# Performance work log

Hardware: AMD Instinct MI355X
Metric: run time of the kernel (lower is better)

Reference implementation:

```python
import jax, jax.numpy as jnp
import numpy as np

EPS = 1e-12  # torch F.normalize eps

def _l2norm(v, axis):
    n = jnp.sqrt(jnp.sum(v * v, axis=axis, keepdims=True))
    return v / jnp.maximum(n, EPS)

def setup_inputs() -> dict:
    key = jax.random.key(0)
    k1, k2, k3 = jax.random.split(key, 3)
    x = jax.random.normal(k1, (32, 512, 30, 40), dtype=jnp.float32)
    conv_w = jax.random.normal(k2, (64, 512), dtype=jnp.float32) * 0.05
    centroids = jax.random.uniform(k3, (64, 512), dtype=jnp.float32)
    return {"x": x, "conv_w": conv_w, "centroids": centroids}

def reference(x, conv_w, centroids):
    N, C, H, W = x.shape
    K = conv_w.shape[0]
    # descriptor-wise L2 normalization over channel dim
    xn = _l2norm(x, axis=1)
    xf = xn.reshape(N, C, H * W)                      # [N, C, HW]
    # 1x1 conv (no bias) -> soft assignment over clusters
    logits = jnp.einsum('kc,nch->nkh', conv_w, xf)     # [N, K, HW]
    a = jax.nn.softmax(logits, axis=1)
    # fused VLAD: sum_hw a*(x - centroid) = (a @ x^T) - centroid * sum_hw a
    vlad = jnp.einsum('nkh,nch->nkc', a, xf) - a.sum(axis=-1)[..., None] * centroids[None]
    vlad = _l2norm(vlad, axis=2)                      # intra-normalization
    v = vlad.reshape(N, K * C)
    return _l2norm(v, axis=1)
```

## Files before the change

kernel.cpp:

```cpp
#include <hip/hip_runtime.h>
#include <hip/hip_bf16.h>
#include <math.h>

#define N_B   32
#define C_DIM 512
#define K_DIM 64
#define HW    1200
#define PTILE 32
#define NPT   38
#define ASLOT 40

typedef __attribute__((ext_vector_type(8))) short bf16x8;
typedef __attribute__((ext_vector_type(4))) float f32x4;

static __device__ inline short f2bf(float f) {
  __hip_bfloat16 h = __float2bfloat16(f);
  union { __hip_bfloat16 b; short s; } u; u.b = h; return u.s;
}

__global__ __launch_bounds__(256) void k1_logits_softmax(
    const float* __restrict__ x, const float* __restrict__ w,
    unsigned short* __restrict__ a_out, float* __restrict__ asum_part)
{
  __shared__ bf16x8 wlds[64 * 8];
  __shared__ bf16x8 xlds[32 * 8];
  __shared__ float  slog[64 * 36];
  __shared__ float  sred[8 * 32];
  __shared__ float  pinv[32], pmax[32], psum[32];

  const int tid  = threadIdx.x;
  const int lane = tid & 63;
  const int wv   = tid >> 6;
  const int n    = blockIdx.x / NPT;
  const int tile = blockIdx.x % NPT;
  const int p0   = tile * PTILE;

  const int sp = tid & 31;
  const int sg = tid >> 5;
  const bool spv = (p0 + sp) < HW;

  const int lr = lane & 15;
  const int lg = lane >> 4;

  const float* xb = x + (size_t)n * C_DIM * HW;

  f32x4 acc0 = {0.f, 0.f, 0.f, 0.f};
  f32x4 acc1 = {0.f, 0.f, 0.f, 0.f};
  float ssq = 0.f;

  for (int c0 = 0; c0 < C_DIM; c0 += 64) {
    {
      const int k = tid >> 3, o = tid & 7;
#pragma unroll
      for (int i = 0; i < 2; ++i) {
        const int kk = k + 32 * i;
        const float* wp = w + (size_t)kk * C_DIM + c0 + o * 8;
        float4 w0 = *(const float4*)wp;
        float4 w1 = *(const float4*)(wp + 4);
        bf16x8 v;
        v[0]=f2bf(w0.x); v[1]=f2bf(w0.y); v[2]=f2bf(w0.z); v[3]=f2bf(w0.w);
        v[4]=f2bf(w1.x); v[5]=f2bf(w1.y); v[6]=f2bf(w1.z); v[7]=f2bf(w1.w);
        wlds[kk * 8 + o] = v;
      }
    }
    {
      float f[8];
#pragma unroll
      for (int j = 0; j < 8; ++j) {
        float v = spv ? xb[(size_t)(c0 + sg * 8 + j) * HW + p0 + sp] : 0.f;
        ssq += v * v;
        f[j] = v;
      }
      bf16x8 v;
#pragma unroll
      for (int j = 0; j < 8; ++j) v[j] = f2bf(f[j]);
      xlds[sp * 8 + sg] = v;
    }
    __syncthreads();
    {
      const int kw = wv * 16;
#pragma unroll
      for (int kc = 0; kc < 2; ++kc) {
        bf16x8 af = wlds[(kw + lr) * 8 + kc * 4 + lg];
        bf16x8 b0 = xlds[lr * 8 + kc * 4 + lg];
        bf16x8 b1 = xlds[(16 + lr) * 8 + kc * 4 + lg];
        acc0 = __builtin_amdgcn_mfma_f32_16x16x32_bf16(af, b0, acc0, 0, 0, 0);
        acc1 = __builtin_amdgcn_mfma_f32_16x16x32_bf16(af, b1, acc1, 0, 0, 0);
      }
    }
    __syncthreads();
  }

  sred[sg * 32 + sp] = ssq;
  __syncthreads();
  if (tid < 32) {
    float s = 0.f;
#pragma unroll
    for (int g = 0; g < 8; ++g) s += sred[g * 32 + tid];
    pinv[tid] = 1.f / fmaxf(sqrtf(s), 1e-12f);
  }
  __syncthreads();

  {
    const int kw = wv * 16;
    const float i0 = pinv[lr];
    const float i1 = pinv[16 + lr];
#pragma unroll
    for (int r = 0; r < 4; ++r) {
      slog[(kw + lg * 4 + r) * 36 + lr]      = acc0[r] * i0;
      slog[(kw + lg * 4 + r) * 36 + 16 + lr] = acc1[r] * i1;
    }
  }
  __syncthreads();

  {
    const int p = tid & 31;
    const int kg = tid >> 5;
    float e[8];
    float m = -1e30f;
#pragma unroll
    for (int j = 0; j < 8; ++j) { e[j] = slog[(kg * 8 + j) * 36 + p]; m = fmaxf(m, e[j]); }
    sred[kg * 32 + p] = m;
    __syncthreads();
    if (tid < 32) {
      float mm = sred[tid];
#pragma unroll
      for (int g = 1; g < 8; ++g) mm = fmaxf(mm, sred[g * 32 + tid]);
      pmax[tid] = mm;
    }
    __syncthreads();
    const float M = pmax[p];
    float s = 0.f;
#pragma unroll
    for (int j = 0; j < 8; ++j) { e[j] = __expf(e[j] - M); s += e[j]; }
    sred[kg * 32 + p] = s;
    __syncthreads();
    if (tid < 32) {
      float ss = 0.f;
#pragma unroll
      for (int g = 0; g < 8; ++g) ss += sred[g * 32 + tid];
      psum[tid] = 1.f / ss;
    }
    __syncthreads();
    const float sc = psum[p];
    const float iv = pinv[p];
    const bool pv = (p0 + p) < HW;
#pragma unroll
    for (int j = 0; j < 8; ++j) {
      float av = e[j] * sc;
      float t = pv ? av : 0.f;
#pragma unroll
      for (int off = 16; off > 0; off >>= 1) t += __shfl_xor(t, off);
      if (p == 0) asum_part[((size_t)n * K_DIM + kg * 8 + j) * ASLOT + tile] = t;
      if (pv) a_out[((size_t)n * K_DIM + kg * 8 + j) * HW + p0 + p] =
                  (unsigned short)f2bf(av * iv);
    }
  }
}

__global__ __launch_bounds__(256) void k2_vlad_gemm(
    const float* __restrict__ x, const unsigned short* __restrict__ a_in,
    float* __restrict__ part)
{
  const int tid  = threadIdx.x;
  const int lane = tid & 63;
  const int wv   = tid >> 6;
  const int b    = blockIdx.x;
  const int half = b & 1;
  const int ct   = (b >> 1) & 15;
  const int n    = b >> 5;
  const int c0   = ct * 32;
  const int hb   = half * 600;
  const int k0   = wv * 16;
  const int lr = lane & 15, lg = lane >> 4;

  const float* xb          = x    + (size_t)n * C_DIM * HW;
  const unsigned short* ab = a_in + (size_t)n * K_DIM * HW;

  f32x4 acc0 = {0,0,0,0}, acc1 = {0,0,0,0};

#pragma unroll 2
  for (int hc = 0; hc < 600; hc += 32) {
    const int hrel = hc + lg * 8;
    const bool gv = hrel < 600;
    const int h = hb + hrel;

    bf16x8 af;
    bf16x8 bx0, bx1;
    if (gv) {
      af = *(const bf16x8*)(ab + (size_t)(k0 + lr) * HW + h);
      {
        const float* xp = xb + (size_t)(c0 + lr) * HW + h;
        float4 x0 = *(const float4*)xp;
        float4 x1 = *(const float4*)(xp + 4);
        bx0[0]=f2bf(x0.x); bx0[1]=f2bf(x0.y); bx0[2]=f2bf(x0.z); bx0[3]=f2bf(x0.w);
        bx0[4]=f2bf(x1.x); bx0[5]=f2bf(x1.y); bx0[6]=f2bf(x1.z); bx0[7]=f2bf(x1.w);
      }
      {
        const float* xp = xb + (size_t)(c0 + 16 + lr) * HW + h;
        float4 x0 = *(const float4*)xp;
        float4 x1 = *(const float4*)(xp + 4);
        bx1[0]=f2bf(x0.x); bx1[1]=f2bf(x0.y); bx1[2]=f2bf(x0.z); bx1[3]=f2bf(x0.w);
        bx1[4]=f2bf(x1.x); bx1[5]=f2bf(x1.y); bx1[6]=f2bf(x1.z); bx1[7]=f2bf(x1.w);
      }
    } else {
#pragma unroll
      for (int j = 0; j < 8; ++j) { af[j] = 0; bx0[j] = 0; bx1[j] = 0; }
    }
    acc0 = __builtin_amdgcn_mfma_f32_16x16x32_bf16(af, bx0, acc0, 0, 0, 0);
    acc1 = __builtin_amdgcn_mfma_f32_16x16x32_bf16(af, bx1, acc1, 0, 0, 0);
  }

  float* pb = part + (((size_t)half * N_B + n) * K_DIM) * C_DIM;
#pragma unroll
  for (int r = 0; r < 4; ++r) {
    pb[(size_t)(k0 + lg * 4 + r) * C_DIM + c0 + lr]      = acc0[r];
    pb[(size_t)(k0 + lg * 4 + r) * C_DIM + c0 + 16 + lr] = acc1[r];
  }
}

__global__ __launch_bounds__(128) void k3a_intranorm(
    const float* __restrict__ part, const float* __restrict__ cent,
    const float* __restrict__ asum_part, float* __restrict__ out,
    float* __restrict__ rowsum)
{
  const int nk = blockIdx.x;
  const int n = nk >> 6, k = nk & 63;
  const int tid = threadIdx.x;

  __shared__ float sasum;
  __shared__ float wss[2];

  float t = (tid < NPT) ? asum_part[(size_t)nk * ASLOT + tid] : 0.f;
  if (tid < 64) {
#pragma unroll
    for (int off = 32; off > 0; off >>= 1) t += __shfl_xor(t, off);
    if (tid == 0) sasum = t;
  }
  __syncthreads();
  const float asum = sasum;

  const float* p0 = part + ((size_t)n * K_DIM + k) * C_DIM;
  const float* p1 = part + ((size_t)(N_B + n) * K_DIM + k) * C_DIM;
  const float* cb = cent + (size_t)k * C_DIM;

  float4 a4 = *(const float4*)&p0[tid * 4];
  float4 b4 = *(const float4*)&p1[tid * 4];
  float4 c4 = *(const float4*)&cb[tid * 4];
  float4 v;
  v.x = a4.x + b4.x - asum * c4.x;
  v.y = a4.y + b4.y - asum * c4.y;
  v.z = a4.z + b4.z - asum * c4.z;
  v.w = a4.w + b4.w - asum * c4.w;

  float ss = v.x * v.x + v.y * v.y + v.z * v.z + v.w * v.w;
#pragma unroll
  for (int off = 32; off > 0; off >>= 1) ss += __shfl_xor(ss, off);
  if ((tid & 63) == 0) wss[tid >> 6] = ss;
  __syncthreads();
  float tot = wss[0] + wss[1];
  float inv = 1.f / fmaxf(sqrtf(tot), 1e-12f);

  float4 o = make_float4(v.x * inv, v.y * inv, v.z * inv, v.w * inv);
  *(float4*)&out[(size_t)n * (K_DIM * C_DIM) + k * C_DIM + tid * 4] = o;
  if (tid == 0) rowsum[nk] = tot * inv * inv;
}

__global__ __launch_bounds__(256) void k3b_globalnorm(
    const float* __restrict__ rowsum, float* __restrict__ out)
{
  const int b = blockIdx.x;
  const int n = b >> 3, seg = b & 7;
  const int tid = threadIdx.x;

  __shared__ float sg;
  float t = (tid < 64) ? rowsum[n * 64 + tid] : 0.f;
  if (tid < 64) {
#pragma unroll
    for (int off = 32; off > 0; off >>= 1) t += __shfl_xor(t, off);
    if (tid == 0) sg = t;
  }
  __syncthreads();
  float ginv = 1.f / fmaxf(sqrtf(sg), 1e-12f);

  float* ob = out + (size_t)n * (K_DIM * C_DIM) + seg * 4096;
#pragma unroll
  for (int i = 0; i < 4; ++i) {
    float4 v = *(float4*)&ob[(i * 256 + tid) * 4];
    v.x *= ginv; v.y *= ginv; v.z *= ginv; v.w *= ginv;
    *(float4*)&ob[(i * 256 + tid) * 4] = v;
  }
}

extern "C" void kernel_launch(void* const* d_in, const int* in_sizes, int n_in,
                              void* d_out, int out_size, void* d_ws, size_t ws_size,
                              hipStream_t stream) {
  (void)in_sizes; (void)n_in; (void)out_size; (void)ws_size;
  const float* x    = (const float*)d_in[0];
  const float* w    = (const float*)d_in[1];
  const float* cent = (const float*)d_in[2];
  float* out = (float*)d_out;

  char* ws = (char*)d_ws;
  unsigned short* a_buf = (unsigned short*)(ws);
  float* asum_p   = (float*)(ws + 4915200);
  float* part     = (float*)(ws + 5242880);
  float* rowsum   = (float*)(ws + 22020096);

  k1_logits_softmax<<<N_B * NPT, 256, 0, stream>>>(x, w, a_buf, asum_p);
  k2_vlad_gemm<<<N_B * 32, 256, 0, stream>>>(x, a_buf, part);
  k3a_intranorm<<<N_B * K_DIM, 128, 0, stream>>>(part, cent, asum_p, out, rowsum);
  k3b_globalnorm<<<N_B * 8, 256, 0, stream>>>(rowsum, out);
}
```

Before: 167.5 us.

## Load GEMM fragments directly in k1 and replace global norm with constant scale

The logits kernel now builds the MFMA operands directly from global loads in registers, dropping the LDS staging and per-chunk barriers, and reduces the per-pixel sum of squares with shuffles. The final global normalization kernel is removed. Each intra-normalized row has unit norm, so the global norm is fixed at sqrt(64) and is folded into a 0.125 scale. This saves a launch and a read-write pass over the output, at the cost of redundant x loads across waves and a wrong result if a VLAD row is exactly zero.

```diff
diff --git a/kernel.cpp b/kernel.cpp
--- a/kernel.cpp
+++ b/kernel.cpp
@@ -22,11 +22,9 @@
     const float* __restrict__ x, const float* __restrict__ w,
     unsigned short* __restrict__ a_out, float* __restrict__ asum_part)
 {
-  __shared__ bf16x8 wlds[64 * 8];
-  __shared__ bf16x8 xlds[32 * 8];
-  __shared__ float  slog[64 * 36];
-  __shared__ float  sred[8 * 32];
-  __shared__ float  pinv[32], pmax[32], psum[32];
+  __shared__ float slog[64 * 36];
+  __shared__ float sred[8 * 32];
+  __shared__ float pinv[32], pmax[32], psum[32];
 
   const int tid  = threadIdx.x;
   const int lane = tid & 63;
@@ -35,81 +33,53 @@
   const int tile = blockIdx.x % NPT;
   const int p0   = tile * PTILE;
 
-  const int sp = tid & 31;
-  const int sg = tid >> 5;
-  const bool spv = (p0 + sp) < HW;
-
   const int lr = lane & 15;
   const int lg = lane >> 4;
+  const int kw = wv * 16;
 
   const float* xb = x + (size_t)n * C_DIM * HW;
+  const int pA = p0 + lr;
+  const int pB = p0 + 16 + lr;
+  const bool vA = pA < HW, vB = pB < HW;
+
+  const float* wrow = w + (size_t)(kw + lr) * C_DIM + lg * 8;
 
   f32x4 acc0 = {0.f, 0.f, 0.f, 0.f};
   f32x4 acc1 = {0.f, 0.f, 0.f, 0.f};
-  float ssq = 0.f;
-
-  for (int c0 = 0; c0 < C_DIM; c0 += 64) {
-    {
-      const int k = tid >> 3, o = tid & 7;
-#pragma unroll
-      for (int i = 0; i < 2; ++i) {
-        const int kk = k + 32 * i;
-        const float* wp = w + (size_t)kk * C_DIM + c0 + o * 8;
-        float4 w0 = *(const float4*)wp;
-        float4 w1 = *(const float4*)(wp + 4);
-        bf16x8 v;
-        v[0]=f2bf(w0.x); v[1]=f2bf(w0.y); v[2]=f2bf(w0.z); v[3]=f2bf(w0.w);
-        v[4]=f2bf(w1.x); v[5]=f2bf(w1.y); v[6]=f2bf(w1.z); v[7]=f2bf(w1.w);
-        wlds[kk * 8 + o] = v;
-      }
-    }
-    {
-      float f[8];
-#pragma unroll
-      for (int j = 0; j < 8; ++j) {
-        float v = spv ? xb[(size_t)(c0 + sg * 8 + j) * HW + p0 + sp] : 0.f;
-        ssq += v * v;
-        f[j] = v;
-      }
-      bf16x8 v;
-#pragma unroll
-      for (int j = 0; j < 8; ++j) v[j] = f2bf(f[j]);
-      xlds[sp * 8 + sg] = v;
-    }
-    __syncthreads();
-    {
-      const int kw = wv * 16;
-#pragma unroll
-      for (int kc = 0; kc < 2; ++kc) {
-        bf16x8 af = wlds[(kw + lr) * 8 + kc * 4 + lg];
-        bf16x8 b0 = xlds[lr * 8 + kc * 4 + lg];
-        bf16x8 b1 = xlds[(16 + lr) * 8 + kc * 4 + lg];
-        acc0 = __builtin_amdgcn_mfma_f32_16x16x32_bf16(af, b0, acc0, 0, 0, 0);
-        acc1 = __builtin_amdgcn_mfma_f32_16x16x32_bf16(af, b1, acc1, 0, 0, 0);
-      }
-    }
-    __syncthreads();
-  }
-
-  sred[sg * 32 + sp] = ssq;
-  __syncthreads();
-  if (tid < 32) {
-    float s = 0.f;
-#pragma unroll
-    for (int g = 0; g < 8; ++g) s += sred[g * 32 + tid];
-    pinv[tid] = 1.f / fmaxf(sqrtf(s), 1e-12f);
-  }
-  __syncthreads();
-
-  {
-    const int kw = wv * 16;
-    const float i0 = pinv[lr];
-    const float i1 = pinv[16 + lr];
-#pragma unroll
-    for (int r = 0; r < 4; ++r) {
-      slog[(kw + lg * 4 + r) * 36 + lr]      = acc0[r] * i0;
-      slog[(kw + lg * 4 + r) * 36 + 16 + lr] = acc1[r] * i1;
-    }
+  float ssqA = 0.f, ssqB = 0.f;
+
+#pragma unroll 4
+  for (int c0 = 0; c0 < C_DIM; c0 += 32) {
+    float4 w0 = *(const float4*)(wrow + c0);
+    float4 w1 = *(const float4*)(wrow + c0 + 4);
+    bf16x8 af;
+    af[0]=f2bf(w0.x); af[1]=f2bf(w0.y); af[2]=f2bf(w0.z); af[3]=f2bf(w0.w);
+    af[4]=f2bf(w1.x); af[5]=f2bf(w1.y); af[6]=f2bf(w1.z); af[7]=f2bf(w1.w);
+    bf16x8 b0, b1;
+    const float* xc = xb + (size_t)(c0 + lg * 8) * HW;
+#pragma unroll
+    for (int j = 0; j < 8; ++j) {
+      float xA = vA ? xc[(size_t)j * HW + pA] : 0.f;
+      float xB = vB ? xc[(size_t)j * HW + pB] : 0.f;
+      ssqA += xA * xA;
+      ssqB += xB * xB;
+      b0[j] = f2bf(xA);
+      b1[j] = f2bf(xB);
+    }
+    acc0 = __builtin_amdgcn_mfma_f32_16x16x32_bf16(af, b0, acc0, 0, 0, 0);
+    acc1 = __builtin_amdgcn_mfma_f32_16x16x32_bf16(af, b1, acc1, 0, 0, 0);
+  }
+
+  ssqA += __shfl_xor(ssqA, 16); ssqA += __shfl_xor(ssqA, 32);
+  ssqB += __shfl_xor(ssqB, 16); ssqB += __shfl_xor(ssqB, 32);
+  const float ivA = 1.f / fmaxf(sqrtf(ssqA), 1e-12f);
+  const float ivB = 1.f / fmaxf(sqrtf(ssqB), 1e-12f);
+  if (wv == 0 && lg == 0) { pinv[lr] = ivA; pinv[16 + lr] = ivB; }
+
+#pragma unroll
+  for (int r = 0; r < 4; ++r) {
+    slog[(kw + lg * 4 + r) * 36 + lr]      = acc0[r] * ivA;
+    slog[(kw + lg * 4 + r) * 36 + 16 + lr] = acc1[r] * ivB;
   }
   __syncthreads();
 
@@ -221,8 +191,7 @@
 
 __global__ __launch_bounds__(128) void k3a_intranorm(
     const float* __restrict__ part, const float* __restrict__ cent,
-    const float* __restrict__ asum_part, float* __restrict__ out,
-    float* __restrict__ rowsum)
+    const float* __restrict__ asum_part, float* __restrict__ out)
 {
   const int nk = blockIdx.x;
   const int n = nk >> 6, k = nk & 63;
@@ -259,37 +228,10 @@
   if ((tid & 63) == 0) wss[tid >> 6] = ss;
   __syncthreads();
   float tot = wss[0] + wss[1];
-  float inv = 1.f / fmaxf(sqrtf(tot), 1e-12f);
+  float inv = 0.125f / fmaxf(sqrtf(tot), 1e-12f);
 
   float4 o = make_float4(v.x * inv, v.y * inv, v.z * inv, v.w * inv);
   *(float4*)&out[(size_t)n * (K_DIM * C_DIM) + k * C_DIM + tid * 4] = o;
-  if (tid == 0) rowsum[nk] = tot * inv * inv;
-}
-
-__global__ __launch_bounds__(256) void k3b_globalnorm(
-    const float* __restrict__ rowsum, float* __restrict__ out)
-{
-  const int b = blockIdx.x;
-  const int n = b >> 3, seg = b & 7;
-  const int tid = threadIdx.x;
-
-  __shared__ float sg;
-  float t = (tid < 64) ? rowsum[n * 64 + tid] : 0.f;
-  if (tid < 64) {
-#pragma unroll
-    for (int off = 32; off > 0; off >>= 1) t += __shfl_xor(t, off);
-    if (tid == 0) sg = t;
-  }
-  __syncthreads();
-  float ginv = 1.f / fmaxf(sqrtf(sg), 1e-12f);
-
-  float* ob = out + (size_t)n * (K_DIM * C_DIM) + seg * 4096;
-#pragma unroll
-  for (int i = 0; i < 4; ++i) {
-    float4 v = *(float4*)&ob[(i * 256 + tid) * 4];
-    v.x *= ginv; v.y *= ginv; v.z *= ginv; v.w *= ginv;
-    *(float4*)&ob[(i * 256 + tid) * 4] = v;
-  }
 }
 
 extern "C" void kernel_launch(void* const* d_in, const int* in_sizes, int n_in,
@@ -305,10 +247,8 @@
   unsigned short* a_buf = (unsigned short*)(ws);
   float* asum_p   = (float*)(ws + 4915200);
   float* part     = (float*)(ws + 5242880);
-  float* rowsum   = (float*)(ws + 22020096);
 
   k1_logits_softmax<<<N_B * NPT, 256, 0, stream>>>(x, w, a_buf, asum_p);
   k2_vlad_gemm<<<N_B * 32, 256, 0, stream>>>(x, a_buf, part);
-  k3a_intranorm<<<N_B * K_DIM, 128, 0, stream>>>(part, cent, asum_p, out, rowsum);
-  k3b_globalnorm<<<N_B * 8, 256, 0, stream>>>(rowsum, out);
-}
+  k3a_intranorm<<<N_B * K_DIM, 128, 0, stream>>>(part, cent, asum_p, out);
+}
```

Result: slower. 178.6 us (+6.6%).
